# Optimization experiments

Hardware: AMD Instinct MI355X
Metric: run time of the kernel (lower is better)

Reference implementation:

```python
import jax, jax.numpy as jnp
import numpy as np

B, N, M, DIN, H = 8, 2048, 2048, 512, 256
SCALE = float(np.sqrt(H))


def _lin_params(key, din, dout):
    kw, kb = jax.random.split(key)
    lim = 1.0 / np.sqrt(din)
    W = jax.random.uniform(kw, (din, dout), jnp.float32, -lim, lim)
    b = jax.random.uniform(kb, (dout,), jnp.float32, -lim, lim)
    return W, b


def setup_inputs() -> dict:
    key = jax.random.key(0)
    ks = jax.random.split(key, 16)
    inp = {
        "q_fp": jax.random.normal(ks[0], (B, N, DIN), jnp.float32),
        "v_ret": jax.random.normal(ks[1], (B, M, DIN), jnp.float32),
        "pi_star": jax.random.uniform(ks[2], (B, N, M), jnp.float32),
    }
    names = ["qs", "ks", "vs", "qe", "ke", "ve"]
    for i, nm in enumerate(names):
        W, b = _lin_params(ks[3 + i], DIN, H)
        inp[f"W{nm}"], inp[f"b{nm}"] = W, b
    inp["W1"], inp["b1"] = _lin_params(ks[10], 4 * H, H)
    inp["W2"], inp["b2"] = _lin_params(ks[11], H, H)
    inp["gamma"] = jnp.ones((1,), jnp.float32)
    inp["ew"] = jnp.array(1.0, jnp.float32)
    return inp


def _forward(q_fp, v_ret, pi_star, Wqs, bqs, Wks, bks, Wvs, bvs,
             Wqe, bqe, Wke, bke, Wve, bve, W1, b1, W2, b2, gamma, ew):
    q_struct = q_fp @ Wqs + bqs          # [B,N,H]
    k_struct = v_ret @ Wks + bks         # [B,M,H]
    v_struct = v_ret @ Wvs + bvs
    q_elec = q_fp @ Wqe + bqe
    k_elec = v_ret @ Wke + bke
    v_elec = v_ret @ Wve + bve

    structural_logits = jnp.einsum("bnh,bmh->bnm", q_struct, k_struct) / SCALE

    # cdist(p=2) via the quadratic expansion, clamped for numeric safety
    q2 = jnp.sum(q_elec * q_elec, -1, keepdims=True)          # [B,N,1]
    k2 = jnp.sum(k_elec * k_elec, -1, keepdims=True)          # [B,M,1]
    d2 = q2 + jnp.swapaxes(k2, -2, -1) - 2.0 * jnp.einsum("bnh,bmh->bnm", q_elec, k_elec)
    electronic_distance = jnp.sqrt(jnp.maximum(d2, 1e-12))    # [B,N,M]
    electronic_scale = jnp.maximum(
        electronic_distance.mean(axis=(-2, -1), keepdims=True), 1e-4)
    electronic_logits = -(electronic_distance / electronic_scale)

    pi_mask = gamma * jnp.log(jnp.maximum(pi_star, 1e-9))
    final_logits = structural_logits + ew * electronic_logits + pi_mask
    attn = jax.nn.softmax(final_logits, axis=-1)              # [B,N,M]

    ctx_s = jnp.einsum("bnm,bmh->bnh", attn, v_struct)
    ctx_e = jnp.einsum("bnm,bmh->bnh", attn, v_elec)
    fused = jnp.concatenate([ctx_s, ctx_e, ctx_s - ctx_e, ctx_s * ctx_e], axis=-1)
    h = jax.nn.silu(fused @ W1 + b1)
    return h @ W2 + b2


def reference(q_fp, v_ret, pi_star, Wqs, bqs, Wks, bks, Wvs, bvs,
              Wqe, bqe, Wke, bke, Wve, bve, W1, b1, W2, b2, gamma, ew):
    return _forward(q_fp, v_ret, pi_star, Wqs, bqs, Wks, bks, Wvs, bvs,
                    Wqe, bqe, Wke, bke, Wve, bve, W1, b1, W2, b2, gamma, ew)
```

## Files before the change

kernel.cpp:

```cpp
#include <hip/hip_runtime.h>

#define Bsz 8
#define Nq  2048
#define Mk  2048
#define BKt 32
#define BUFE (128 * BKt)

typedef __attribute__((ext_vector_type(8))) short   short8;
typedef __attribute__((ext_vector_type(4))) float   floatx4;

__device__ __forceinline__ unsigned short f2bf(float f) {
  union { float f; unsigned u; } x; x.f = f;
  unsigned r = x.u + 0x7fffu + ((x.u >> 16) & 1u);
  return (unsigned short)(r >> 16);
}
__device__ __forceinline__ float bf2f(unsigned short s) {
  union { unsigned u; float f; } x; x.u = ((unsigned)s) << 16;
  return x.f;
}

__device__ __forceinline__ void gload16(const unsigned short* g, unsigned short* l) {
  __builtin_amdgcn_global_load_lds(
      (const __attribute__((address_space(1))) void*)g,
      (__attribute__((address_space(3))) void*)l, 16, 0, 0);
}

__device__ __forceinline__ void gemm_core8_nt(
    const unsigned short* __restrict__ A, int lda,
    const unsigned short* __restrict__ B, int ldb,
    int K, unsigned short* ldsA, unsigned short* ldsB,
    floatx4 (&acc)[4][2])
{
  const int tid  = threadIdx.x;
  const int lane = tid & 63;
  const int wid  = tid >> 6;
  const int wm   = wid & 1;
  const int wn   = wid >> 1;
  const int fr   = lane & 15;
  const int fk   = (lane >> 4) << 3;
  const int lr   = lane >> 2;
  const int lc   = (lane & 3) << 3;
  const int r0   = wid << 4;

  const unsigned short* gA = A + (size_t)(r0 + lr) * lda + lc;
  const unsigned short* gB = B + (size_t)(r0 + lr) * ldb + lc;
  unsigned short* lA = ldsA + r0 * BKt;
  unsigned short* lB = ldsB + r0 * BKt;
  const unsigned short* fa = ldsA + (wm * 64 + fr) * BKt + fk;
  const unsigned short* fb = ldsB + (wn * 32 + fr) * BKt + fk;

  gload16(gA, lA); gA += BKt;
  gload16(gB, lB); gB += BKt;
  __syncthreads();

  int cur = 0;
  for (int k0 = 0; k0 < K; k0 += BKt) {
    const int nxt = cur ^ 1;
    if (k0 + BKt < K) {
      gload16(gA, lA + nxt * BUFE); gA += BKt;
      gload16(gB, lB + nxt * BUFE); gB += BKt;
    }
    const unsigned short* fac = fa + cur * BUFE;
    const unsigned short* fbc = fb + cur * BUFE;
    short8 af[4], bfr[2];
#pragma unroll
    for (int i = 0; i < 4; i++) af[i]  = *(const short8*)(fac + i * 16 * BKt);
#pragma unroll
    for (int j = 0; j < 2; j++) bfr[j] = *(const short8*)(fbc + j * 16 * BKt);
#pragma unroll
    for (int i = 0; i < 4; i++)
#pragma unroll
      for (int j = 0; j < 2; j++)
        acc[i][j] = __builtin_amdgcn_mfma_f32_16x16x32_bf16(af[i], bfr[j], acc[i][j], 0, 0, 0);
    __syncthreads();
    cur = nxt;
  }
}

#define EPILOGUE_VARS \
  const int lane = threadIdx.x & 63; \
  const int wid  = threadIdx.x >> 6; \
  const int wm   = wid & 1; \
  const int wn   = wid >> 1; \
  const int r4   = (lane >> 4) * 4;  \
  const int cn   = lane & 15; \
  (void)wid;

__global__ __launch_bounds__(512, 4) void k_proj(
    const float* __restrict__ A, const unsigned short* __restrict__ Bw,
    const float* __restrict__ bias, unsigned short* __restrict__ Cout,
    int Ncols, int K)
{
  __shared__ alignas(16) unsigned short ldsA[2 * BUFE];
  __shared__ alignas(16) unsigned short ldsB[2 * BUFE];
  floatx4 acc[4][2];
#pragma unroll
  for (int i = 0; i < 4; i++)
#pragma unroll
    for (int j = 0; j < 2; j++)
#pragma unroll
      for (int t = 0; t < 4; t++) acc[i][j][t] = 0.f;

  const int tid  = threadIdx.x;
  const int lane = tid & 63;
  const int wid  = tid >> 6;
  const int wm   = wid & 1;
  const int wn   = wid >> 1;
  const int fr   = lane & 15;
  const int fk   = (lane >> 4) << 3;
  const int lr   = lane >> 2;
  const int lc   = (lane & 3) << 3;
  const int r0   = wid << 4;

  const float* ap = A + ((size_t)blockIdx.x * 128 + r0 + lr) * K + lc;
  const unsigned short* gB = Bw + ((size_t)blockIdx.y * 128 + r0 + lr) * K + lc;
  unsigned short* lB = ldsB + r0 * BKt;
  unsigned short* sa = ldsA + (r0 + lr) * BKt + lc;
  const unsigned short* fa = ldsA + (wm * 64 + fr) * BKt + fk;
  const unsigned short* fb = ldsB + (wn * 32 + fr) * BKt + fk;

  {
    float4 f0 = *(const float4*)(ap);
    float4 f1 = *(const float4*)(ap + 4);
    ap += BKt;
    uint4 pa;
    pa.x = f2bf(f0.x) | ((unsigned)f2bf(f0.y) << 16);
    pa.y = f2bf(f0.z) | ((unsigned)f2bf(f0.w) << 16);
    pa.z = f2bf(f1.x) | ((unsigned)f2bf(f1.y) << 16);
    pa.w = f2bf(f1.z) | ((unsigned)f2bf(f1.w) << 16);
    gload16(gB, lB); gB += BKt;
    *(uint4*)sa = pa;
  }
  __syncthreads();

  int cur = 0;
  for (int k0 = 0; k0 < K; k0 += BKt) {
    const int nxt = cur ^ 1;
    const bool more = (k0 + BKt < K);
    float4 n0, n1;
    if (more) {
      n0 = *(const float4*)(ap);
      n1 = *(const float4*)(ap + 4);
      ap += BKt;
      gload16(gB, lB + nxt * BUFE); gB += BKt;
    }
    const unsigned short* fac = fa + cur * BUFE;
    const unsigned short* fbc = fb + cur * BUFE;
    short8 af[4], bfr[2];
#pragma unroll
    for (int i = 0; i < 4; i++) af[i]  = *(const short8*)(fac + i * 16 * BKt);
#pragma unroll
    for (int j = 0; j < 2; j++) bfr[j] = *(const short8*)(fbc + j * 16 * BKt);
#pragma unroll
    for (int i = 0; i < 4; i++)
#pragma unroll
      for (int j = 0; j < 2; j++)
        acc[i][j] = __builtin_amdgcn_mfma_f32_16x16x32_bf16(af[i], bfr[j], acc[i][j], 0, 0, 0);
    if (more) {
      uint4 pa;
      pa.x = f2bf(n0.x) | ((unsigned)f2bf(n0.y) << 16);
      pa.y = f2bf(n0.z) | ((unsigned)f2bf(n0.w) << 16);
      pa.z = f2bf(n1.x) | ((unsigned)f2bf(n1.y) << 16);
      pa.w = f2bf(n1.z) | ((unsigned)f2bf(n1.w) << 16);
      *(uint4*)(sa + nxt * BUFE) = pa;
    }
    __syncthreads();
    cur = nxt;
  }

  const int r4 = (lane >> 4) * 4;
  const int cn = lane & 15;
#pragma unroll
  for (int i = 0; i < 4; i++) {
#pragma unroll
    for (int j = 0; j < 2; j++) {
      int gc = blockIdx.y * 128 + wn * 32 + j * 16 + cn;
      float bv = bias[gc];
#pragma unroll
      for (int r = 0; r < 4; r++) {
        int gr = blockIdx.x * 128 + wm * 64 + i * 16 + r4 + r;
        Cout[(size_t)gr * Ncols + gc] = f2bf(acc[i][j][r] + bv);
      }
    }
  }
}

template<int MODE>
__global__ __launch_bounds__(512, 4) void k_gemm_bias(
    const unsigned short* __restrict__ A, const unsigned short* __restrict__ Bw,
    const float* __restrict__ bias, void* __restrict__ Cout, int Ncols, int K)
{
  __shared__ alignas(16) unsigned short ldsA[2 * BUFE];
  __shared__ alignas(16) unsigned short ldsB[2 * BUFE];
  floatx4 acc[4][2];
#pragma unroll
  for (int i = 0; i < 4; i++)
#pragma unroll
    for (int j = 0; j < 2; j++)
#pragma unroll
      for (int t = 0; t < 4; t++) acc[i][j][t] = 0.f;

  const unsigned short* Ab = A + (size_t)blockIdx.x * 128 * K;
  const unsigned short* Bb = Bw + (size_t)blockIdx.y * 128 * K;
  gemm_core8_nt(Ab, K, Bb, K, K, ldsA, ldsB, acc);

  EPILOGUE_VARS
#pragma unroll
  for (int i = 0; i < 4; i++) {
#pragma unroll
    for (int j = 0; j < 2; j++) {
      int gc = blockIdx.y * 128 + wn * 32 + j * 16 + cn;
      float bv = bias[gc];
#pragma unroll
      for (int r = 0; r < 4; r++) {
        int gr = blockIdx.x * 128 + wm * 64 + i * 16 + r4 + r;
        float v = acc[i][j][r] + bv;
        if constexpr (MODE == 1) v = v / (1.f + __expf(-v));
        if constexpr (MODE == 2)
          ((float*)Cout)[(size_t)gr * Ncols + gc] = v;
        else
          ((unsigned short*)Cout)[(size_t)gr * Ncols + gc] = f2bf(v);
      }
    }
  }
}

__global__ __launch_bounds__(512, 4) void k_sd(
    const unsigned short* __restrict__ Xq, const unsigned short* __restrict__ Xk,
    const float* __restrict__ q2, const float* __restrict__ k2,
    int b0, float* __restrict__ dsum, unsigned* __restrict__ sd)
{
  __shared__ alignas(16) unsigned short ldsAs[2 * BUFE];
  __shared__ alignas(16) unsigned short ldsAe[2 * BUFE];
  __shared__ alignas(16) unsigned short ldsBs[2 * BUFE];
  __shared__ alignas(16) unsigned short ldsBe[2 * BUFE];
  floatx4 accS[4][2], accE[4][2];
#pragma unroll
  for (int i = 0; i < 4; i++)
#pragma unroll
    for (int j = 0; j < 2; j++)
#pragma unroll
      for (int t = 0; t < 4; t++) { accS[i][j][t] = 0.f; accE[i][j][t] = 0.f; }

  const int z = blockIdx.z;
  const int b = b0 + z;

  const int tid  = threadIdx.x;
  const int lane = tid & 63;
  const int wid  = tid >> 6;
  const int wm   = wid & 1;
  const int wn   = wid >> 1;
  const int fr   = lane & 15;
  const int fk   = (lane >> 4) << 3;
  const int lr   = lane >> 2;
  const int lc   = (lane & 3) << 3;
  const int r0   = wid << 4;

  const unsigned short* gAs = Xq + ((size_t)(b * Nq) + blockIdx.x * 128 + r0 + lr) * 512 + lc;
  const unsigned short* gAe = gAs + 256;
  const unsigned short* gBs = Xk + ((size_t)(b * Mk) + blockIdx.y * 128 + r0 + lr) * 1024 + lc;
  const unsigned short* gBe = gBs + 512;
  unsigned short* lAs = ldsAs + r0 * BKt;
  unsigned short* lAe = ldsAe + r0 * BKt;
  unsigned short* lBs = ldsBs + r0 * BKt;
  unsigned short* lBe = ldsBe + r0 * BKt;
  const unsigned short* fas = ldsAs + (wm * 64 + fr) * BKt + fk;
  const unsigned short* fae = ldsAe + (wm * 64 + fr) * BKt + fk;
  const unsigned short* fbs = ldsBs + (wn * 32 + fr) * BKt + fk;
  const unsigned short* fbe = ldsBe + (wn * 32 + fr) * BKt + fk;

  gload16(gAs, lAs); gAs += BKt;
  gload16(gAe, lAe); gAe += BKt;
  gload16(gBs, lBs); gBs += BKt;
  gload16(gBe, lBe); gBe += BKt;
  __syncthreads();

  int cur = 0;
  for (int k0 = 0; k0 < 256; k0 += BKt) {
    const int nxt = cur ^ 1;
    if (k0 + BKt < 256) {
      gload16(gAs, lAs + nxt * BUFE); gAs += BKt;
      gload16(gAe, lAe + nxt * BUFE); gAe += BKt;
      gload16(gBs, lBs + nxt * BUFE); gBs += BKt;
      gload16(gBe, lBe + nxt * BUFE); gBe += BKt;
    }
    {
      short8 af[4], bfr[2];
      const unsigned short* fac = fas + cur * BUFE;
      const unsigned short* fbc = fbs + cur * BUFE;
#pragma unroll
      for (int i = 0; i < 4; i++) af[i]  = *(const short8*)(fac + i * 16 * BKt);
#pragma unroll
      for (int j = 0; j < 2; j++) bfr[j] = *(const short8*)(fbc + j * 16 * BKt);
#pragma unroll
      for (int i = 0; i < 4; i++)
#pragma unroll
        for (int j = 0; j < 2; j++)
          accS[i][j] = __builtin_amdgcn_mfma_f32_16x16x32_bf16(af[i], bfr[j], accS[i][j], 0, 0, 0);
    }
    {
      short8 af[4], bfr[2];
      const unsigned short* fac = fae + cur * BUFE;
      const unsigned short* fbc = fbe + cur * BUFE;
#pragma unroll
      for (int i = 0; i < 4; i++) af[i]  = *(const short8*)(fac + i * 16 * BKt);
#pragma unroll
      for (int j = 0; j < 2; j++) bfr[j] = *(const short8*)(fbc + j * 16 * BKt);
#pragma unroll
      for (int i = 0; i < 4; i++)
#pragma unroll
        for (int j = 0; j < 2; j++)
          accE[i][j] = __builtin_amdgcn_mfma_f32_16x16x32_bf16(af[i], bfr[j], accE[i][j], 0, 0, 0);
    }
    __syncthreads();
    cur = nxt;
  }

  const int r4 = (lane >> 4) * 4;
  const int cn = lane & 15;
  const int colT = blockIdx.y * 128 + wn * 32;
  const float kk0 = k2[b * Mk + colT + cn];
  const float kk1 = k2[b * Mk + colT + 16 + cn];

  float lsum = 0.f;
#pragma unroll
  for (int i = 0; i < 4; i++) {
#pragma unroll
    for (int r = 0; r < 4; r++) {
      const int n = blockIdx.x * 128 + wm * 64 + i * 16 + r4 + r;
      const float qq = q2[b * Nq + n];
      unsigned* srow = sd + (size_t)(z * Nq + n) * Mk;
#pragma unroll
      for (int j = 0; j < 2; j++) {
        const int m = colT + j * 16 + cn;
        float d = sqrtf(fmaxf(qq + (j ? kk1 : kk0) - 2.f * accE[i][j][r], 1e-12f));
        lsum += d;
        srow[m] = (unsigned)f2bf(accS[i][j][r] * 0.0625f)
                | ((unsigned)f2bf(d) << 16);
      }
    }
  }
#pragma unroll
  for (int o = 32; o; o >>= 1) lsum += __shfl_down(lsum, o);
  __syncthreads();
  float* red = (float*)ldsAs;
  if (lane == 0) red[wid] = lsum;
  __syncthreads();
  if (threadIdx.x == 0) {
    float s = 0.f;
#pragma unroll
    for (int t = 0; t < 8; t++) s += red[t];
    atomicAdd(dsum + b, s);
  }
}

__global__ __launch_bounds__(256) void k_softmax(
    const unsigned* __restrict__ sd, const float* __restrict__ pi,
    const float* __restrict__ dsum, const float* __restrict__ gamma_p,
    const float* __restrict__ ew_p, int b0,
    unsigned short* __restrict__ attn, float* __restrict__ rowsum)
{
  const int wid  = threadIdx.x >> 6;
  const int lane = threadIdx.x & 63;
  const int rl   = blockIdx.x * 4 + wid;
  const int b    = b0 + (rl >> 11);
  const int n    = rl & 2047;

  const float scale = fmaxf(dsum[b] * (1.f / (2048.f * 2048.f)), 1e-4f);
  const float einv  = ew_p[0] / scale;
  const float gv    = gamma_p[0];
  const bool  g1    = (gv == 1.0f);

  const unsigned*  sp = sd  + (size_t)rl * Mk;
  const float*     pp = pi  + ((size_t)b * Nq + n) * Mk;
  unsigned short*  ap = attn + ((size_t)b * Nq + n) * Mk;

  float rs = 0.f;
  for (int it = 0; it < 8; ++it) {
    const int c = it * 256 + lane * 4;
    const uint4  sv = *(const uint4*)(sp + c);
    const float4 pv = *(const float4*)(pp + c);
    const unsigned uu[4]  = {sv.x, sv.y, sv.z, sv.w};
    const float    pp4[4] = {pv.x, pv.y, pv.z, pv.w};
    float e[4];
#pragma unroll
    for (int t = 0; t < 4; ++t) {
      union { unsigned u; float f; } cs, cd;
      cs.u = uu[t] << 16;
      cd.u = uu[t] & 0xffff0000u;
      float p  = fmaxf(pp4[t], 1e-9f);
      float pf = g1 ? p : __expf(gv * __logf(p));
      e[t] = __expf(cs.f - einv * cd.f) * pf;
      rs += e[t];
    }
    uint2 st;
    st.x = (unsigned)f2bf(e[0]) | ((unsigned)f2bf(e[1]) << 16);
    st.y = (unsigned)f2bf(e[2]) | ((unsigned)f2bf(e[3]) << 16);
    *(uint2*)(ap + c) = st;
  }
#pragma unroll
  for (int o = 32; o; o >>= 1) rs += __shfl_down(rs, o);
  if (lane == 0) rowsum[b * Nq + n] = rs;
}

__global__ __launch_bounds__(512, 4) void k_pv(
    const unsigned short* __restrict__ At, const unsigned short* __restrict__ VT,
    const float* __restrict__ rowsum, unsigned short* __restrict__ ctx)
{
  __shared__ alignas(16) unsigned short ldsA[2 * BUFE];
  __shared__ alignas(16) unsigned short ldsB[2 * BUFE];
  floatx4 acc[4][2];
#pragma unroll
  for (int i = 0; i < 4; i++)
#pragma unroll
    for (int j = 0; j < 2; j++)
#pragma unroll
      for (int t = 0; t < 4; t++) acc[i][j][t] = 0.f;

  const int l  = blockIdx.x;
  const int lg = ((l & 7) << 3) | (l >> 3);
  const int tx = lg >> 2;
  const int ty = lg & 3;
  const int b  = blockIdx.z;
  const unsigned short* Ab = At + ((size_t)b * Nq + tx * 128) * (size_t)Mk;
  const unsigned short* Bb = VT + ((size_t)b * 512 + ty * 128) * (size_t)Mk;
  gemm_core8_nt(Ab, Mk, Bb, Mk, Mk, ldsA, ldsB, acc);

  EPILOGUE_VARS
  const int rowbase = b * Nq + tx * 128 + wm * 64;
#pragma unroll
  for (int i = 0; i < 4; i++) {
    float rinv[4];
#pragma unroll
    for (int r = 0; r < 4; r++)
      rinv[r] = 1.f / rowsum[rowbase + i * 16 + r4 + r];
#pragma unroll
    for (int j = 0; j < 2; j++) {
      int gc = ty * 128 + wn * 32 + j * 16 + cn;
#pragma unroll
      for (int r = 0; r < 4; r++) {
        int gr = tx * 128 + wm * 64 + i * 16 + r4 + r;
        ctx[((size_t)b * Nq + gr) * 512 + gc] = f2bf(acc[i][j][r] * rinv[r]);
      }
    }
  }
}

__global__ void k_prep_w(
    const float* __restrict__ Wqs, const float* __restrict__ Wqe,
    const float* __restrict__ Wks, const float* __restrict__ Wvs,
    const float* __restrict__ Wke, const float* __restrict__ Wve,
    const float* __restrict__ W1,  const float* __restrict__ W2,
    const float* __restrict__ bqs, const float* __restrict__ bqe,
    const float* __restrict__ bks, const float* __restrict__ bvs,
    const float* __restrict__ bke, const float* __restrict__ bve,
    unsigned short* __restrict__ WqT, unsigned short* __restrict__ WkT,
    unsigned short* __restrict__ W1T, unsigned short* __restrict__ W2T,
    float* __restrict__ bq, float* __restrict__ bk, float* __restrict__ dsum)
{
  int gid = blockIdx.x * 256 + threadIdx.x;
  int idx = gid;
  if (idx < 512 * 512) {
    int j = idx >> 9, k = idx & 511;
    float v = (j < 256) ? Wqs[k * 256 + j] : Wqe[k * 256 + (j - 256)];
    WqT[idx] = f2bf(v);
  } else if ((idx -= 512 * 512) < 1024 * 512) {
    int j = idx >> 9, k = idx & 511;
    int s = j >> 8, jj = j & 255;
    const float* Wp = (s == 0) ? Wks : (s == 1) ? Wvs : (s == 2) ? Wke : Wve;
    WkT[idx] = f2bf(Wp[k * 256 + jj]);
  } else if ((idx -= 1024 * 512) < 256 * 1024) {
    int j = idx >> 10, k = idx & 1023;
    W1T[idx] = f2bf(W1[k * 256 + j]);
  } else if ((idx -= 256 * 1024) < 256 * 256) {
    int j = idx >> 8, k = idx & 255;
    W2T[idx] = f2bf(W2[k * 256 + j]);
  }
  if (gid < 512)  bq[gid] = (gid < 256) ? bqs[gid] : bqe[gid - 256];
  if (gid < 1024) bk[gid] = (gid < 256) ? bks[gid]
                    : (gid < 512) ? bvs[gid - 256]
                    : (gid < 768) ? bke[gid - 512] : bve[gid - 768];
  if (gid < 8) dsum[gid] = 0.f;
}

__global__ __launch_bounds__(256) void k_rowsq(
    const unsigned short* __restrict__ X, int stride, int colOff, float* __restrict__ out)
{
  int row = blockIdx.x * 4 + (threadIdx.x >> 6);
  int lane = threadIdx.x & 63;
  const unsigned short* p = X + (size_t)row * stride + colOff + lane * 4;
  uint2 u = *(const uint2*)p;
  float a0 = bf2f((unsigned short)(u.x & 0xffff));
  float a1 = bf2f((unsigned short)(u.x >> 16));
  float a2 = bf2f((unsigned short)(u.y & 0xffff));
  float a3 = bf2f((unsigned short)(u.y >> 16));
  float s = a0 * a0 + a1 * a1 + a2 * a2 + a3 * a3;
#pragma unroll
  for (int o = 32; o; o >>= 1) s += __shfl_down(s, o);
  if (lane == 0) out[row] = s;
}

__global__ void k_trans_vt(const unsigned short* __restrict__ Xk, unsigned short* __restrict__ VT) {
  __shared__ unsigned short t[32][33];
  const int b = blockIdx.z;
  const int m0 = blockIdx.x * 32, j0 = blockIdx.y * 32;
  const int tx = threadIdx.x, ty = threadIdx.y;
#pragma unroll
  for (int i = 0; i < 4; i++) {
    int m = m0 + ty + i * 8;
    int j = j0 + tx;
    int c = (j < 256) ? (256 + j) : (512 + j);
    t[ty + i * 8][tx] = Xk[((size_t)b * Mk + m) * 1024 + c];
  }
  __syncthreads();
#pragma unroll
  for (int i = 0; i < 4; i++) {
    int j = j0 + ty + i * 8;
    int m = m0 + tx;
    VT[((size_t)b * 512 + j) * Mk + m] = t[tx][ty + i * 8];
  }
}

__global__ void k_fused(const unsigned short* __restrict__ ctx, unsigned short* __restrict__ fused) {
  int idx = blockIdx.x * 256 + threadIdx.x;
  int bn = idx >> 8;
  int j = idx & 255;
  float cs = bf2f(ctx[(size_t)bn * 512 + j]);
  float ce = bf2f(ctx[(size_t)bn * 512 + 256 + j]);
  size_t o = (size_t)bn * 1024 + j;
  fused[o]       = f2bf(cs);
  fused[o + 256] = f2bf(ce);
  fused[o + 512] = f2bf(cs - ce);
  fused[o + 768] = f2bf(cs * ce);
}

extern "C" void kernel_launch(void* const* d_in, const int* in_sizes, int n_in,
                              void* d_out, int out_size, void* d_ws, size_t ws_size,
                              hipStream_t stream) {
  (void)in_sizes; (void)n_in; (void)out_size; (void)ws_size;
  const float* q_fp  = (const float*)d_in[0];
  const float* v_ret = (const float*)d_in[1];
  const float* pi    = (const float*)d_in[2];
  const float* Wqs = (const float*)d_in[3];  const float* bqs = (const float*)d_in[4];
  const float* Wks = (const float*)d_in[5];  const float* bks = (const float*)d_in[6];
  const float* Wvs = (const float*)d_in[7];  const float* bvs = (const float*)d_in[8];
  const float* Wqe = (const float*)d_in[9];  const float* bqe = (const float*)d_in[10];
  const float* Wke = (const float*)d_in[11]; const float* bke = (const float*)d_in[12];
  const float* Wve = (const float*)d_in[13]; const float* bve = (const float*)d_in[14];
  const float* W1  = (const float*)d_in[15]; const float* b1  = (const float*)d_in[16];
  const float* W2  = (const float*)d_in[17]; const float* b2  = (const float*)d_in[18];
  const float* gamma = (const float*)d_in[19];
  const float* ew    = (const float*)d_in[20];

  char* w = (char*)d_ws;
  unsigned short* WqT = (unsigned short*)(w + 0);
  unsigned short* WkT = (unsigned short*)(w + 524288);
  unsigned short* W1T = (unsigned short*)(w + 1572864);
  unsigned short* W2T = (unsigned short*)(w + 2097152);
  float* bq   = (float*)(w + 2228224);
  float* bk   = (float*)(w + 2230272);
  float* q2   = (float*)(w + 2234368);
  float* k2   = (float*)(w + 2299904);
  float* dsum = (float*)(w + 2365440);
  unsigned short* ctx  = (unsigned short*)(w + 2365696);
  unsigned short* hbuf = (unsigned short*)(w + 19142912);
  unsigned short* Xq = (unsigned short*)(w + 35920128);
  unsigned short* Xk = (unsigned short*)(w + 52697344);
  unsigned short* VT = (unsigned short*)(w + 86251776);
  unsigned short* attn = (unsigned short*)(w + 103028992);
  unsigned short* fused = attn;
  unsigned* sdbuf = (unsigned*)(w + 2365696);
  float* rowsum = (float*)d_out;

  k_prep_w<<<4352, 256, 0, stream>>>(Wqs, Wqe, Wks, Wvs, Wke, Wve, W1, W2,
                                     bqs, bqe, bks, bvs, bke, bve,
                                     WqT, WkT, W1T, W2T, bq, bk, dsum);
  k_proj<<<dim3(128, 4), 512, 0, stream>>>(q_fp,  WqT, bq, Xq, 512, 512);
  k_proj<<<dim3(128, 8), 512, 0, stream>>>(v_ret, WkT, bk, Xk, 1024, 512);
  k_rowsq<<<4096, 256, 0, stream>>>(Xq, 512, 256, q2);
  k_rowsq<<<4096, 256, 0, stream>>>(Xk, 1024, 512, k2);
  for (int c = 0; c < 4; ++c) {
    k_sd<<<dim3(16, 16, 2), 512, 0, stream>>>(Xq, Xk, q2, k2, 2 * c, dsum, sdbuf);
    k_softmax<<<1024, 256, 0, stream>>>(sdbuf, pi, dsum, gamma, ew, 2 * c,
                                        attn, rowsum);
  }
  k_trans_vt<<<dim3(64, 16, 8), dim3(32, 8), 0, stream>>>(Xk, VT);
  k_pv<<<dim3(64, 1, 8), 512, 0, stream>>>(attn, VT, rowsum, ctx);
  k_fused<<<16384, 256, 0, stream>>>(ctx, fused);
  k_gemm_bias<1><<<dim3(128, 2), 512, 0, stream>>>(fused, W1T, b1, hbuf, 256, 1024);
  k_gemm_bias<2><<<dim3(128, 2), 512, 0, stream>>>(hbuf, W2T, b2, d_out, 256, 256);
}
```

Measured before the change: 571.7 us.

## Fuse softmax exponentiation with PV matmul and fused-feature epilogue

Replaces the separate softmax kernel, the attention-times-V GEMM and the fused-feature kernel with one kernel. It computes the exponentiated logits per 32-row stripe into double-buffered LDS and feeds them straight into MFMA against V, then normalises and writes the concatenated fused features directly. This avoids writing and re-reading the full bf16 attention matrix and the ctx buffer, and removes two launches. In exchange, B operands are loaded straight from global memory without LDS staging, and only 256 blocks with small row tiles are launched per chunk, so V is re-read once per stripe and occupancy may be low. Chunking also changes from four batches of two to two batches of four.

```diff
diff --git a/kernel.cpp b/kernel.cpp
--- a/kernel.cpp
+++ b/kernel.cpp
@@ -354,94 +354,138 @@
   }
 }
 
-__global__ __launch_bounds__(256) void k_softmax(
+__global__ __launch_bounds__(512, 2) void k_pvf(
     const unsigned* __restrict__ sd, const float* __restrict__ pi,
+    const unsigned short* __restrict__ VT,
     const float* __restrict__ dsum, const float* __restrict__ gamma_p,
     const float* __restrict__ ew_p, int b0,
-    unsigned short* __restrict__ attn, float* __restrict__ rowsum)
+    unsigned short* __restrict__ fused)
 {
-  const int wid  = threadIdx.x >> 6;
-  const int lane = threadIdx.x & 63;
-  const int rl   = blockIdx.x * 4 + wid;
-  const int b    = b0 + (rl >> 11);
-  const int n    = rl & 2047;
+  __shared__ alignas(16) unsigned short eld[2][32 * 64];
+  __shared__ float rsum[32];
+
+  const int bid    = blockIdx.x;
+  const int z      = bid & 3;
+  const int stripe = bid >> 2;
+  const int b      = b0 + z;
+  const int n0     = stripe * 32;
+
+  const int tid  = threadIdx.x;
+  const int lane = tid & 63;
+  const int wid  = tid >> 6;
+  const int wm   = wid & 1;
+  const int wn   = wid >> 1;
+  const int fr   = lane & 15;
+  const int fk8  = (lane >> 4) << 3;
 
   const float scale = fmaxf(dsum[b] * (1.f / (2048.f * 2048.f)), 1e-4f);
   const float einv  = ew_p[0] / scale;
   const float gv    = gamma_p[0];
   const bool  g1    = (gv == 1.0f);
 
-  const unsigned*  sp = sd  + (size_t)rl * Mk;
-  const float*     pp = pi  + ((size_t)b * Nq + n) * Mk;
-  unsigned short*  ap = attn + ((size_t)b * Nq + n) * Mk;
+  floatx4 acc[8];
+#pragma unroll
+  for (int j = 0; j < 8; ++j)
+#pragma unroll
+    for (int t = 0; t < 4; ++t) acc[j][t] = 0.f;
+
+  const int srow = tid >> 4;
+  const int sm   = (tid & 15) << 2;
+  const unsigned* sp = sd + ((size_t)(z * Nq) + n0 + srow) * (size_t)Mk + sm;
+  const float*    pp = pi + ((size_t)(b * Nq) + n0 + srow) * (size_t)Mk + sm;
+  const int wIdx = (srow * 128 + ((sm * 2) ^ ((srow & 7) << 4))) >> 1;
+
+  const int arow  = wm * 16 + fr;
+  const int aIdx0 = (arow * 128 + ((((lane >> 4) << 4) + 0 ) ^ ((arow & 7) << 4))) >> 1;
+  const int aIdx1 = (arow * 128 + ((((lane >> 4) << 4) + 64) ^ ((arow & 7) << 4))) >> 1;
+
+  const unsigned short* bp[8];
+#pragma unroll
+  for (int j = 0; j < 8; ++j) {
+    const int vrow = (j < 4) ? (wn * 64 + j * 16 + fr)
+                             : (256 + wn * 64 + (j - 4) * 16 + fr);
+    bp[j] = VT + ((size_t)b * 512 + vrow) * (size_t)Mk + fk8;
+  }
 
   float rs = 0.f;
-  for (int it = 0; it < 8; ++it) {
-    const int c = it * 256 + lane * 4;
-    const uint4  sv = *(const uint4*)(sp + c);
-    const float4 pv = *(const float4*)(pp + c);
-    const unsigned uu[4]  = {sv.x, sv.y, sv.z, sv.w};
-    const float    pp4[4] = {pv.x, pv.y, pv.z, pv.w};
-    float e[4];
-#pragma unroll
-    for (int t = 0; t < 4; ++t) {
-      union { unsigned u; float f; } cs, cd;
-      cs.u = uu[t] << 16;
-      cd.u = uu[t] & 0xffff0000u;
-      float p  = fmaxf(pp4[t], 1e-9f);
-      float pf = g1 ? p : __expf(gv * __logf(p));
-      e[t] = __expf(cs.f - einv * cd.f) * pf;
-      rs += e[t];
-    }
-    uint2 st;
-    st.x = (unsigned)f2bf(e[0]) | ((unsigned)f2bf(e[1]) << 16);
-    st.y = (unsigned)f2bf(e[2]) | ((unsigned)f2bf(e[3]) << 16);
-    *(uint2*)(ap + c) = st;
-  }
-#pragma unroll
-  for (int o = 32; o; o >>= 1) rs += __shfl_down(rs, o);
-  if (lane == 0) rowsum[b * Nq + n] = rs;
-}
-
-__global__ __launch_bounds__(512, 4) void k_pv(
-    const unsigned short* __restrict__ At, const unsigned short* __restrict__ VT,
-    const float* __restrict__ rowsum, unsigned short* __restrict__ ctx)
-{
-  __shared__ alignas(16) unsigned short ldsA[2 * BUFE];
-  __shared__ alignas(16) unsigned short ldsB[2 * BUFE];
-  floatx4 acc[4][2];
-#pragma unroll
-  for (int i = 0; i < 4; i++)
-#pragma unroll
-    for (int j = 0; j < 2; j++)
-#pragma unroll
-      for (int t = 0; t < 4; t++) acc[i][j][t] = 0.f;
-
-  const int l  = blockIdx.x;
-  const int lg = ((l & 7) << 3) | (l >> 3);
-  const int tx = lg >> 2;
-  const int ty = lg & 3;
-  const int b  = blockIdx.z;
-  const unsigned short* Ab = At + ((size_t)b * Nq + tx * 128) * (size_t)Mk;
-  const unsigned short* Bb = VT + ((size_t)b * 512 + ty * 128) * (size_t)Mk;
-  gemm_core8_nt(Ab, Mk, Bb, Mk, Mk, ldsA, ldsB, acc);
-
-  EPILOGUE_VARS
-  const int rowbase = b * Nq + tx * 128 + wm * 64;
-#pragma unroll
-  for (int i = 0; i < 4; i++) {
-    float rinv[4];
-#pragma unroll
-    for (int r = 0; r < 4; r++)
-      rinv[r] = 1.f / rowsum[rowbase + i * 16 + r4 + r];
-#pragma unroll
-    for (int j = 0; j < 2; j++) {
-      int gc = ty * 128 + wn * 32 + j * 16 + cn;
-#pragma unroll
-      for (int r = 0; r < 4; r++) {
-        int gr = tx * 128 + wm * 64 + i * 16 + r4 + r;
-        ctx[((size_t)b * Nq + gr) * 512 + gc] = f2bf(acc[i][j][r] * rinv[r]);
+
+#define E_COMPUTE_STORE(SV, PV, BUF) do {                                    \
+    const unsigned uu_[4] = {(SV).x, (SV).y, (SV).z, (SV).w};                \
+    const float    pf_[4] = {(PV).x, (PV).y, (PV).z, (PV).w};                \
+    float e_[4];                                                             \
+    _Pragma("unroll")                                                        \
+    for (int t_ = 0; t_ < 4; ++t_) {                                         \
+      union { unsigned u; float f; } cs_, cd_;                               \
+      cs_.u = uu_[t_] << 16;                                                 \
+      cd_.u = uu_[t_] & 0xffff0000u;                                         \
+      float p_  = fmaxf(pf_[t_], 1e-9f);                                     \
+      float pw_ = g1 ? p_ : __expf(gv * __logf(p_));                         \
+      e_[t_] = __expf(cs_.f - einv * cd_.f) * pw_;                           \
+      rs += e_[t_];                                                          \
+    }                                                                        \
+    uint2 st_;                                                               \
+    st_.x = (unsigned)f2bf(e_[0]) | ((unsigned)f2bf(e_[1]) << 16);           \
+    st_.y = (unsigned)f2bf(e_[2]) | ((unsigned)f2bf(e_[3]) << 16);           \
+    *(uint2*)(&eld[BUF][wIdx]) = st_;                                        \
+  } while (0)
+
+  uint4  sv = *(const uint4*)sp;  sp += 64;
+  float4 pv = *(const float4*)pp; pp += 64;
+  E_COMPUTE_STORE(sv, pv, 0);
+  uint4  svn = *(const uint4*)sp;  sp += 64;
+  float4 pvn = *(const float4*)pp; pp += 64;
+  __syncthreads();
+
+  int cur = 0;
+  for (int t = 0; t < 32; ++t) {
+    short8 af0 = *(const short8*)(&eld[cur][aIdx0]);
+    short8 af1 = *(const short8*)(&eld[cur][aIdx1]);
+#pragma unroll
+    for (int j = 0; j < 8; ++j) {
+      short8 bf0 = *(const short8*)(bp[j]);
+      acc[j] = __builtin_amdgcn_mfma_f32_16x16x32_bf16(af0, bf0, acc[j], 0, 0, 0);
+    }
+#pragma unroll
+    for (int j = 0; j < 8; ++j) {
+      short8 bf1 = *(const short8*)(bp[j] + 32);
+      acc[j] = __builtin_amdgcn_mfma_f32_16x16x32_bf16(af1, bf1, acc[j], 0, 0, 0);
+      bp[j] += 64;
+    }
+    if (t < 31) {
+      E_COMPUTE_STORE(svn, pvn, cur ^ 1);
+      if (t < 30) {
+        svn = *(const uint4*)sp;  sp += 64;
+        pvn = *(const float4*)pp; pp += 64;
       }
+    }
+    __syncthreads();
+    cur ^= 1;
+  }
+#undef E_COMPUTE_STORE
+
+  rs += __shfl_xor(rs, 1);
+  rs += __shfl_xor(rs, 2);
+  rs += __shfl_xor(rs, 4);
+  rs += __shfl_xor(rs, 8);
+  if ((tid & 15) == 0) rsum[srow] = rs;
+  __syncthreads();
+
+  const int r4 = (lane >> 4) * 4;
+  const int cn = lane & 15;
+#pragma unroll
+  for (int rr = 0; rr < 4; ++rr) {
+    const int row = wm * 16 + r4 + rr;
+    const float rinv = 1.f / rsum[row];
+    unsigned short* out = fused + ((size_t)(b * Nq) + n0 + row) * 1024;
+#pragma unroll
+    for (int j = 0; j < 4; ++j) {
+      const int col = wn * 64 + j * 16 + cn;
+      const float cs = acc[j][rr] * rinv;
+      const float ce = acc[j + 4][rr] * rinv;
+      out[col]       = f2bf(cs);
+      out[col + 256] = f2bf(ce);
+      out[col + 512] = f2bf(cs - ce);
+      out[col + 768] = f2bf(cs * ce);
     }
   }
 }
@@ -521,19 +565,6 @@
   }
 }
 
-__global__ void k_fused(const unsigned short* __restrict__ ctx, unsigned short* __restrict__ fused) {
-  int idx = blockIdx.x * 256 + threadIdx.x;
-  int bn = idx >> 8;
-  int j = idx & 255;
-  float cs = bf2f(ctx[(size_t)bn * 512 + j]);
-  float ce = bf2f(ctx[(size_t)bn * 512 + 256 + j]);
-  size_t o = (size_t)bn * 1024 + j;
-  fused[o]       = f2bf(cs);
-  fused[o + 256] = f2bf(ce);
-  fused[o + 512] = f2bf(cs - ce);
-  fused[o + 768] = f2bf(cs * ce);
-}
-
 extern "C" void kernel_launch(void* const* d_in, const int* in_sizes, int n_in,
                               void* d_out, int out_size, void* d_ws, size_t ws_size,
                               hipStream_t stream) {
@@ -562,15 +593,12 @@
   float* q2   = (float*)(w + 2234368);
   float* k2   = (float*)(w + 2299904);
   float* dsum = (float*)(w + 2365440);
-  unsigned short* ctx  = (unsigned short*)(w + 2365696);
-  unsigned short* hbuf = (unsigned short*)(w + 19142912);
+  unsigned short* fused = (unsigned short*)(w + 2365696);
   unsigned short* Xq = (unsigned short*)(w + 35920128);
   unsigned short* Xk = (unsigned short*)(w + 52697344);
   unsigned short* VT = (unsigned short*)(w + 86251776);
-  unsigned short* attn = (unsigned short*)(w + 103028992);
-  unsigned short* fused = attn;
-  unsigned* sdbuf = (unsigned*)(w + 2365696);
-  float* rowsum = (float*)d_out;
+  unsigned* sdbuf = (unsigned*)(w + 103028992);
+  unsigned short* hbuf = (unsigned short*)(w + 103028992);
 
   k_prep_w<<<4352, 256, 0, stream>>>(Wqs, Wqe, Wks, Wvs, Wke, Wve, W1, W2,
                                      bqs, bqe, bks, bvs, bke, bve,
@@ -579,14 +607,11 @@
   k_proj<<<dim3(128, 8), 512, 0, stream>>>(v_ret, WkT, bk, Xk, 1024, 512);
   k_rowsq<<<4096, 256, 0, stream>>>(Xq, 512, 256, q2);
   k_rowsq<<<4096, 256, 0, stream>>>(Xk, 1024, 512, k2);
-  for (int c = 0; c < 4; ++c) {
-    k_sd<<<dim3(16, 16, 2), 512, 0, stream>>>(Xq, Xk, q2, k2, 2 * c, dsum, sdbuf);
-    k_softmax<<<1024, 256, 0, stream>>>(sdbuf, pi, dsum, gamma, ew, 2 * c,
-                                        attn, rowsum);
-  }
   k_trans_vt<<<dim3(64, 16, 8), dim3(32, 8), 0, stream>>>(Xk, VT);
-  k_pv<<<dim3(64, 1, 8), 512, 0, stream>>>(attn, VT, rowsum, ctx);
-  k_fused<<<16384, 256, 0, stream>>>(ctx, fused);
+  for (int c = 0; c < 2; ++c) {
+    k_sd<<<dim3(16, 16, 4), 512, 0, stream>>>(Xq, Xk, q2, k2, 4 * c, dsum, sdbuf);
+    k_pvf<<<256, 512, 0, stream>>>(sdbuf, pi, VT, dsum, gamma, ew, 4 * c, fused);
+  }
   k_gemm_bias<1><<<dim3(128, 2), 512, 0, stream>>>(fused, W1T, b1, hbuf, 256, 1024);
   k_gemm_bias<2><<<dim3(128, 2), 512, 0, stream>>>(hbuf, W2T, b2, d_out, 256, 256);
 }
```

Measured after the change: 786.4 us. 1.38x slower.
